# Kernel optimization log

Hardware: AMD Instinct MI355X
Metric: run time of the kernel (lower is better)

## Reference

```python
import jax, jax.numpy as jnp
import numpy as np

EPS = 1e-5

def _layernorm(x, g, b):
    mu = jnp.mean(x, axis=-1, keepdims=True)
    var = jnp.mean(jnp.square(x - mu), axis=-1, keepdims=True)
    return (x - mu) * jax.lax.rsqrt(var + EPS) * g + b

def setup_inputs() -> dict:
    key = jax.random.key(0)
    ks = jax.random.split(key, 8)
    F, N, C, H = 4096, 64, 256, 8
    x = jax.random.normal(ks[0], (F, N, C), dtype=jnp.float32)
    adj = jax.random.randint(ks[1], (N, N), 0, 2, dtype=jnp.int32)
    adj = jnp.maximum(adj, jnp.eye(N, dtype=jnp.int32))  # self-loops: no empty rows
    s = 1.0 / np.sqrt(C)
    w_qkv = jax.random.normal(ks[2], (C, 3 * C), dtype=jnp.float32) * s
    w1 = jax.random.normal(ks[3], (C, C), dtype=jnp.float32) * s
    b1 = jnp.zeros((C,), dtype=jnp.float32)
    w2 = jax.random.normal(ks[4], (C, C), dtype=jnp.float32) * s
    b2 = jnp.zeros((C,), dtype=jnp.float32)
    ln1_g = jnp.ones((C,), jnp.float32); ln1_b = jnp.zeros((C,), jnp.float32)
    ln2_g = jnp.ones((C,), jnp.float32); ln2_b = jnp.zeros((C,), jnp.float32)
    return {"x": x, "adj": adj, "w_qkv": w_qkv, "ln1_g": ln1_g, "ln1_b": ln1_b,
            "ln2_g": ln2_g, "ln2_b": ln2_b, "w1": w1, "b1": b1, "w2": w2, "b2": b2}

def reference(x, adj, w_qkv, ln1_g, ln1_b, ln2_g, ln2_b, w1, b1, w2, b2):
    F, N, C = x.shape
    H = 8
    D = C // H
    # fused QKV projection (bias-free, as in lin_qkv)
    qkv = jnp.einsum('fnc,ck->fnk', x, w_qkv)
    q, k, v = jnp.split(qkv, 3, axis=-1)
    q = q.reshape(F, N, H, D)
    k = k.reshape(F, N, H, D)
    v = v.reshape(F, N, H, D)
    # adjacency-masked attention (dropout in eval mode = identity)
    scores = jnp.einsum('fnhd,fmhd->fhnm', q, k) / jnp.sqrt(jnp.asarray(D, x.dtype))
    mask = (adj > 0)[None, None, :, :]  # [1,1,N,N]
    scores = jnp.where(mask, scores, jnp.asarray(-1e9, x.dtype))
    attn = jax.nn.softmax(scores, axis=-1)
    t = jnp.einsum('fhnm,fmhd->fnhd', attn, v).reshape(F, N, C)
    # add & norm (attention)
    x = _layernorm(x + t, ln1_g, ln1_b)
    # feed-forward: Linear -> ReLU -> Linear
    h = jax.nn.relu(jnp.einsum('fnc,cd->fnd', x, w1) + b1)
    f_out = jnp.einsum('fnd,dc->fnc', h, w2) + b2
    # add & norm (ffn)
    x = _layernorm(x + f_out, ln2_g, ln2_b)
    return x
```

## Files before the change

kernel.cpp:

```cpp
#include <hip/hip_runtime.h>
#include <hip/hip_bf16.h>

#define NN 64
#define NC 256
#define NH 8
#define ND 32

using bf16 = __hip_bfloat16;

typedef __attribute__((ext_vector_type(8))) short bf16x8v;
typedef __attribute__((ext_vector_type(4))) float f32x4;

__device__ __forceinline__ float ld(const float* p, int i) { return p[i]; }
__device__ __forceinline__ float ld(const bf16*  p, int i) { return __bfloat162float(p[i]); }

__device__ __forceinline__ unsigned short bfbits(float f) {
    bf16 h = __float2bfloat16(f);
    return *reinterpret_cast<unsigned short*>(&h);
}
__device__ __forceinline__ unsigned pack2(float lo, float hi) {
    return (unsigned)bfbits(lo) | ((unsigned)bfbits(hi) << 16);
}
__device__ __forceinline__ void st_bf16(void* p, float v) {
    *(unsigned short*)p = bfbits(v);
}
__device__ __forceinline__ float ld_lds_bf16(const void* p) {
    return __uint_as_float((unsigned)(*(const unsigned short*)p) << 16);
}
__device__ __forceinline__ f32x4 MFMA(bf16x8v a, bf16x8v b, f32x4 c) {
    return __builtin_amdgcn_mfma_f32_16x16x32_bf16(a, b, c, 0, 0, 0);
}
__device__ __forceinline__ bf16x8v LD128(const unsigned char* p) {
    return *(const bf16x8v*)p;
}

__device__ __forceinline__ int xs_chunk_byte(int r, int chunk) {
    return (r << 9) + ((chunk ^ (r & 7)) << 4);
}
__device__ __forceinline__ int xs_elem_byte(int r, int c) {
    return (r << 9) + (((c >> 3) ^ (r & 7)) << 4) + ((c & 7) << 1);
}
__device__ __forceinline__ int t128_byte(int base, int r, int chunk) {
    return base + (r << 7) + ((chunk ^ (r & 7)) << 4);
}
__device__ __forceinline__ int t64_byte(int base, int r, int chunk) {
    return base + (r << 6) + ((chunk ^ ((r >> 1) & 3)) << 4);
}
#define WBB 32768
#define VTB 45056
#define PBB 49152
#define QHB 57344
#define KHB 61440

template<typename T>
__device__ __forceinline__ void ldT2x4(const T* g, int stride, uint2& c0, uint2& c1) {
    if constexpr (sizeof(T) == 4) {
        const float* gf = (const float*)g;
        float2 r0 = *(const float2*)(gf);
        float2 r1 = *(const float2*)(gf + stride);
        float2 r2 = *(const float2*)(gf + 2 * stride);
        float2 r3 = *(const float2*)(gf + 3 * stride);
        c0.x = pack2(r0.x, r1.x); c0.y = pack2(r2.x, r3.x);
        c1.x = pack2(r0.y, r1.y); c1.y = pack2(r2.y, r3.y);
    } else {
        unsigned r0 = *(const unsigned*)(g);
        unsigned r1 = *(const unsigned*)(g + stride);
        unsigned r2 = *(const unsigned*)(g + 2 * stride);
        unsigned r3 = *(const unsigned*)(g + 3 * stride);
        c0.x = (r0 & 0xFFFFu) | (r1 << 16);
        c0.y = (r2 & 0xFFFFu) | (r3 << 16);
        c1.x = (r0 >> 16) | (r1 & 0xFFFF0000u);
        c1.y = (r2 >> 16) | (r3 & 0xFFFF0000u);
    }
}

template<typename T>
__device__ __forceinline__ void stage_wq(unsigned char* smem, const T* wqkv,
                                         int h, int k0, int tid) {
    const int jp = tid & 15;
    const int kq = (tid >> 4) * 4;
    #pragma unroll
    for (int sec = 0; sec < 3; ++sec) {
        const T* g = wqkv + (size_t)(k0 + kq) * (3 * NC) + sec * NC + h * ND + jp * 2;
        uint2 c0, c1;
        ldT2x4(g, 3 * NC, c0, c1);
        const int j = sec * 32 + jp * 2;
        const int off = (kq & 7) << 1;
        *(uint2*)(smem + t128_byte(WBB, j,     kq >> 3) + off) = c0;
        *(uint2*)(smem + t128_byte(WBB, j + 1, kq >> 3) + off) = c1;
    }
}

template<typename T>
__device__ __forceinline__ void stage_w(unsigned char* smem, const T* wm, int k0, int tid) {
    const int jp = tid & 127;
    #pragma unroll
    for (int it = 0; it < 4; ++it) {
        const int kq = (tid >> 7) * 4 + it * 8;
        const T* g = wm + (size_t)(k0 + kq) * NC + jp * 2;
        uint2 c0, c1;
        ldT2x4(g, NC, c0, c1);
        const int j = jp * 2;
        const int off = (kq & 7) << 1;
        *(uint2*)(smem + t64_byte(WBB, j,     kq >> 3) + off) = c0;
        *(uint2*)(smem + t64_byte(WBB, j + 1, kq >> 3) + off) = c1;
    }
}

template<typename T>
__device__ __forceinline__ void stage_x(unsigned char* smem, const T* xg, int tid) {
    const int r  = tid >> 2;
    const int c0 = (tid & 3) * 64;
    #pragma unroll
    for (int e = 0; e < 8; ++e) {
        const int c = c0 + e * 8;
        uint4 wv;
        if constexpr (sizeof(T) == 4) {
            const float4* g = (const float4*)((const float*)xg + r * NC + c);
            float4 v0 = g[0], v1 = g[1];
            wv.x = pack2(v0.x, v0.y); wv.y = pack2(v0.z, v0.w);
            wv.z = pack2(v1.x, v1.y); wv.w = pack2(v1.z, v1.w);
        } else {
            wv = *(const uint4*)((const bf16*)xg + r * NC + c);
        }
        *(uint4*)(smem + xs_chunk_byte(r, c >> 3)) = wv;
    }
}

__global__ void detect_dtype_kernel(const unsigned* __restrict__ g, int* __restrict__ flag) {
    *flag = (*g == 0x3F800000u) ? 1 : 0;
}

template <typename T>
__global__ __launch_bounds__(256, 2) void spatial_layer(
    const int* __restrict__ flag, const int want,
    const T* __restrict__ x, const int* __restrict__ adj,
    const T* __restrict__ wqkv,
    const T* __restrict__ ln1g, const T* __restrict__ ln1b,
    const T* __restrict__ ln2g, const T* __restrict__ ln2b,
    const T* __restrict__ w1, const T* __restrict__ fb1,
    const T* __restrict__ w2, const T* __restrict__ fb2,
    T* __restrict__ out)
{
    if (flag && *flag != want) return;

    __shared__ __align__(16) unsigned char smem[65536];

    const int tid = threadIdx.x;
    const int fr  = blockIdx.x;
    const int w   = tid >> 6;
    const int li  = tid & 15;
    const int lg  = (tid >> 4) & 3;

    {
        const uint4 zz = make_uint4(0u, 0u, 0u, 0u);
        uint4* z = (uint4*)smem;
        #pragma unroll
        for (int i = 0; i < 16; ++i) z[tid + 256 * i] = zz;
    }

    const T* xg = x + (size_t)fr * NN * NC;

    unsigned amask = 0;
    #pragma unroll
    for (int r = 0; r < 4; ++r)
        #pragma unroll
        for (int nt = 0; nt < 4; ++nt)
            if (adj[(w * 16 + lg * 4 + r) * NN + nt * 16 + li] > 0)
                amask |= 1u << (r * 4 + nt);

    __syncthreads();
    stage_x(smem, xg, tid);

    const f32x4 z4 = {0.f, 0.f, 0.f, 0.f};
    f32x4 tacc[16];
    #pragma unroll
    for (int i = 0; i < 16; ++i) tacc[i] = z4;

    #pragma unroll
    for (int h = 0; h < NH; ++h) {
        f32x4 acc6[6];
        #pragma unroll
        for (int i = 0; i < 6; ++i) acc6[i] = z4;

        #pragma unroll
        for (int s = 0; s < 4; ++s) {
            __syncthreads();
            stage_wq(smem, wqkv, h, s * 64, tid);
            __syncthreads();
            #pragma unroll
            for (int kk = 0; kk < 2; ++kk) {
                bf16x8v a = LD128(smem + xs_chunk_byte(w * 16 + li, s * 8 + kk * 4 + lg));
                #pragma unroll
                for (int nt = 0; nt < 6; ++nt) {
                    bf16x8v b = LD128(smem + t128_byte(WBB, nt * 16 + li, kk * 4 + lg));
                    acc6[nt] = MFMA(a, b, acc6[nt]);
                }
            }
        }

        #pragma unroll
        for (int nt = 0; nt < 2; ++nt)
            #pragma unroll
            for (int r = 0; r < 4; ++r) {
                const int row = w * 16 + lg * 4 + r;
                const int d   = nt * 16 + li;
                st_bf16(smem + t64_byte(QHB, row, d >> 3) + ((d & 7) << 1),
                        acc6[nt][r] * 0.17677669529663687f);
                st_bf16(smem + t64_byte(KHB, row, d >> 3) + ((d & 7) << 1),
                        acc6[2 + nt][r]);
                st_bf16(smem + t128_byte(VTB, d, row >> 3) + ((row & 7) << 1),
                        acc6[4 + nt][r]);
            }
        __syncthreads();

        {
            bf16x8v aq = LD128(smem + t64_byte(QHB, w * 16 + li, lg));
            f32x4 sc[4];
            #pragma unroll
            for (int nt = 0; nt < 4; ++nt) {
                bf16x8v bk = LD128(smem + t64_byte(KHB, nt * 16 + li, lg));
                sc[nt] = MFMA(aq, bk, z4);
            }
            #pragma unroll
            for (int r = 0; r < 4; ++r) {
                float mx = -1e30f;
                #pragma unroll
                for (int nt = 0; nt < 4; ++nt) {
                    float sv = ((amask >> (r * 4 + nt)) & 1u) ? sc[nt][r] : -1e9f;
                    sc[nt][r] = sv;
                    mx = fmaxf(mx, sv);
                }
                mx = fmaxf(mx, __shfl_xor(mx, 1));
                mx = fmaxf(mx, __shfl_xor(mx, 2));
                mx = fmaxf(mx, __shfl_xor(mx, 4));
                mx = fmaxf(mx, __shfl_xor(mx, 8));
                float sum = 0.f;
                #pragma unroll
                for (int nt = 0; nt < 4; ++nt) {
                    float e = __expf(sc[nt][r] - mx);
                    sc[nt][r] = e;
                    sum += e;
                }
                sum += __shfl_xor(sum, 1);
                sum += __shfl_xor(sum, 2);
                sum += __shfl_xor(sum, 4);
                sum += __shfl_xor(sum, 8);
                const float inv = 1.0f / sum;
                const int row = w * 16 + lg * 4 + r;
                #pragma unroll
                for (int nt = 0; nt < 4; ++nt) {
                    const int col = nt * 16 + li;
                    st_bf16(smem + t128_byte(PBB, row, col >> 3) + ((col & 7) << 1),
                            sc[nt][r] * inv);
                }
            }
        }
        __syncthreads();

        #pragma unroll
        for (int kb = 0; kb < 2; ++kb) {
            bf16x8v ap = LD128(smem + t128_byte(PBB, w * 16 + li, kb * 4 + lg));
            #pragma unroll
            for (int nt = 0; nt < 2; ++nt) {
                bf16x8v bv = LD128(smem + t128_byte(VTB, nt * 16 + li, kb * 4 + lg));
                tacc[h * 2 + nt] = MFMA(ap, bv, tacc[h * 2 + nt]);
            }
        }
    }
    __syncthreads();

    float mus[4], rss[4];
    {
        float s1[4] = {0.f, 0.f, 0.f, 0.f};
        float s2[4] = {0.f, 0.f, 0.f, 0.f};
        #pragma unroll
        for (int cb = 0; cb < 16; ++cb)
            #pragma unroll
            for (int r = 0; r < 4; ++r) {
                const int row = w * 16 + lg * 4 + r;
                const int col = cb * 16 + li;
                float y = tacc[cb][r] + ld_lds_bf16(smem + xs_elem_byte(row, col));
                tacc[cb][r] = y;
                s1[r] += y; s2[r] += y * y;
            }
        #pragma unroll
        for (int r = 0; r < 4; ++r) {
            float a = s1[r], b = s2[r];
            a += __shfl_xor(a, 1); b += __shfl_xor(b, 1);
            a += __shfl_xor(a, 2); b += __shfl_xor(b, 2);
            a += __shfl_xor(a, 4); b += __shfl_xor(b, 4);
            a += __shfl_xor(a, 8); b += __shfl_xor(b, 8);
            const float mu  = a * (1.f / 256.f);
            const float var = b * (1.f / 256.f) - mu * mu;
            mus[r] = mu;
            rss[r] = rsqrtf(var + 1e-5f);
        }
        #pragma unroll
        for (int cb = 0; cb < 16; ++cb) {
            const int col = cb * 16 + li;
            const float g = ld(ln1g, col), be = ld(ln1b, col);
            #pragma unroll
            for (int r = 0; r < 4; ++r) {
                const int row = w * 16 + lg * 4 + r;
                const float x1 = (tacc[cb][r] - mus[r]) * rss[r] * g + be;
                tacc[cb][r] = x1;
                st_bf16(smem + xs_elem_byte(row, col), x1);
            }
        }
    }

    f32x4 facc[16];
    #pragma unroll
    for (int i = 0; i < 16; ++i) facc[i] = z4;
    #pragma unroll
    for (int s = 0; s < 8; ++s) {
        __syncthreads();
        stage_w(smem, w1, s * 32, tid);
        __syncthreads();
        bf16x8v a = LD128(smem + xs_chunk_byte(w * 16 + li, s * 4 + lg));
        #pragma unroll
        for (int nt = 0; nt < 16; ++nt) {
            bf16x8v b = LD128(smem + t64_byte(WBB, nt * 16 + li, lg));
            facc[nt] = MFMA(a, b, facc[nt]);
        }
    }
    #pragma unroll
    for (int nt = 0; nt < 16; ++nt) {
        const int col = nt * 16 + li;
        const float bv = ld(fb1, col);
        #pragma unroll
        for (int r = 0; r < 4; ++r) {
            const int row = w * 16 + lg * 4 + r;
            st_bf16(smem + xs_elem_byte(row, col), fmaxf(facc[nt][r] + bv, 0.f));
        }
    }

    #pragma unroll
    for (int i = 0; i < 16; ++i) facc[i] = z4;
    #pragma unroll
    for (int s = 0; s < 8; ++s) {
        __syncthreads();
        stage_w(smem, w2, s * 32, tid);
        __syncthreads();
        bf16x8v a = LD128(smem + xs_chunk_byte(w * 16 + li, s * 4 + lg));
        #pragma unroll
        for (int nt = 0; nt < 16; ++nt) {
            bf16x8v b = LD128(smem + t64_byte(WBB, nt * 16 + li, lg));
            facc[nt] = MFMA(a, b, facc[nt]);
        }
    }

    {
        float s1[4] = {0.f, 0.f, 0.f, 0.f};
        float s2[4] = {0.f, 0.f, 0.f, 0.f};
        #pragma unroll
        for (int cb = 0; cb < 16; ++cb) {
            const float bv = ld(fb2, cb * 16 + li);
            #pragma unroll
            for (int r = 0; r < 4; ++r) {
                const float y = tacc[cb][r] + facc[cb][r] + bv;
                facc[cb][r] = y;
                s1[r] += y; s2[r] += y * y;
            }
        }
        #pragma unroll
        for (int r = 0; r < 4; ++r) {
            float a = s1[r], b = s2[r];
            a += __shfl_xor(a, 1); b += __shfl_xor(b, 1);
            a += __shfl_xor(a, 2); b += __shfl_xor(b, 2);
            a += __shfl_xor(a, 4); b += __shfl_xor(b, 4);
            a += __shfl_xor(a, 8); b += __shfl_xor(b, 8);
            const float mu  = a * (1.f / 256.f);
            const float var = b * (1.f / 256.f) - mu * mu;
            mus[r] = mu;
            rss[r] = rsqrtf(var + 1e-5f);
        }
        T* og = out + (size_t)fr * NN * NC;
        #pragma unroll
        for (int cb = 0; cb < 16; ++cb) {
            const int col = cb * 16 + li;
            const float g = ld(ln2g, col), be = ld(ln2b, col);
            #pragma unroll
            for (int r = 0; r < 4; ++r) {
                const int row = w * 16 + lg * 4 + r;
                const float yv = (facc[cb][r] - mus[r]) * rss[r] * g + be;
                if constexpr (sizeof(T) == 4) ((float*)og)[row * NC + col] = yv;
                else ((unsigned short*)og)[row * NC + col] = bfbits(yv);
            }
        }
    }
}

extern "C" void kernel_launch(void* const* d_in, const int* in_sizes, int n_in,
                              void* d_out, int out_size, void* d_ws, size_t ws_size,
                              hipStream_t stream) {
    const int F = in_sizes[0] / (NN * NC);

    const int* flag = (ws_size >= 4) ? (const int*)d_ws : nullptr;
    if (flag) {
        detect_dtype_kernel<<<1, 1, 0, stream>>>((const unsigned*)d_in[3], (int*)d_ws);
        spatial_layer<bf16><<<dim3(F), dim3(256), 0, stream>>>(
            flag, 0,
            (const bf16*)d_in[0], (const int*)d_in[1], (const bf16*)d_in[2],
            (const bf16*)d_in[3], (const bf16*)d_in[4],
            (const bf16*)d_in[5], (const bf16*)d_in[6],
            (const bf16*)d_in[7], (const bf16*)d_in[8],
            (const bf16*)d_in[9], (const bf16*)d_in[10],
            (bf16*)d_out);
    }
    spatial_layer<float><<<dim3(F), dim3(256), 0, stream>>>(
        flag, 1,
        (const float*)d_in[0], (const int*)d_in[1], (const float*)d_in[2],
        (const float*)d_in[3], (const float*)d_in[4],
        (const float*)d_in[5], (const float*)d_in[6],
        (const float*)d_in[7], (const float*)d_in[8],
        (const float*)d_in[9], (const float*)d_in[10],
        (float*)d_out);
}
```

Baseline: 1.427 ms.

## Double-buffer weight staging via register prefetch and keep x fragments in registers

Weight tiles for the QKV, FFN1 and FFN2 GEMMs are now loaded from global memory into registers one stage ahead and written into a second LDS buffer after the MFMAs. This overlaps global latency with compute and halves the barriers per stage. The x A-operand fragments and the residual x values are held in registers instead of an LDS tile, which frees LDS for the two weight buffers. The final output is staged through LDS so each thread writes vectorized, coalesced 16-byte stores. In exchange, register pressure rises a lot (xa, xres, rq/rw, tacc, facc) and may spill or reduce occupancy.

```diff
diff --git a/kernel.cpp b/kernel.cpp
--- a/kernel.cpp
+++ b/kernel.cpp
@@ -24,9 +24,8 @@
 __device__ __forceinline__ void st_bf16(void* p, float v) {
     *(unsigned short*)p = bfbits(v);
 }
-__device__ __forceinline__ float ld_lds_bf16(const void* p) {
-    return __uint_as_float((unsigned)(*(const unsigned short*)p) << 16);
-}
+__device__ __forceinline__ float lo2f(unsigned p) { return __uint_as_float(p << 16); }
+__device__ __forceinline__ float hi2f(unsigned p) { return __uint_as_float(p & 0xffff0000u); }
 __device__ __forceinline__ f32x4 MFMA(bf16x8v a, bf16x8v b, f32x4 c) {
     return __builtin_amdgcn_mfma_f32_16x16x32_bf16(a, b, c, 0, 0, 0);
 }
@@ -34,96 +33,122 @@
     return *(const bf16x8v*)p;
 }
 
-__device__ __forceinline__ int xs_chunk_byte(int r, int chunk) {
-    return (r << 9) + ((chunk ^ (r & 7)) << 4);
-}
-__device__ __forceinline__ int xs_elem_byte(int r, int c) {
-    return (r << 9) + (((c >> 3) ^ (r & 7)) << 4) + ((c & 7) << 1);
-}
 __device__ __forceinline__ int t128_byte(int base, int r, int chunk) {
     return base + (r << 7) + ((chunk ^ (r & 7)) << 4);
 }
 __device__ __forceinline__ int t64_byte(int base, int r, int chunk) {
     return base + (r << 6) + ((chunk ^ ((r >> 1) & 3)) << 4);
 }
-#define WBB 32768
-#define VTB 45056
-#define PBB 49152
-#define QHB 57344
-#define KHB 61440
+#define WB(i) ((i) << 14)
+#define VTB 32768
+#define PBB 36864
+#define QHB 45056
+#define KHB 49152
+#define XS2 32768
+__device__ __forceinline__ int xs2_chunk(int r, int c) {
+    return XS2 + (r << 9) + ((c ^ (r & 7)) << 4);
+}
+__device__ __forceinline__ int xs2_elem(int r, int c) {
+    return XS2 + (r << 9) + (((c >> 3) ^ (r & 7)) << 4) + ((c & 7) << 1);
+}
+__device__ __forceinline__ int yf_byte(int r, int c16) {
+    return (r << 10) + ((c16 ^ (r & 7)) << 4);
+}
+
+template<int S> struct RawSel { using type = unsigned; };
+template<> struct RawSel<4>   { using type = float2;   };
+template<typename T> using RawW = typename RawSel<sizeof(T)>::type;
 
 template<typename T>
-__device__ __forceinline__ void ldT2x4(const T* g, int stride, uint2& c0, uint2& c1) {
+__device__ __forceinline__ void raw_load4(const T* g, int stride, RawW<T>* r) {
     if constexpr (sizeof(T) == 4) {
         const float* gf = (const float*)g;
-        float2 r0 = *(const float2*)(gf);
-        float2 r1 = *(const float2*)(gf + stride);
-        float2 r2 = *(const float2*)(gf + 2 * stride);
-        float2 r3 = *(const float2*)(gf + 3 * stride);
-        c0.x = pack2(r0.x, r1.x); c0.y = pack2(r2.x, r3.x);
-        c1.x = pack2(r0.y, r1.y); c1.y = pack2(r2.y, r3.y);
+        r[0] = *(const float2*)(gf);
+        r[1] = *(const float2*)(gf + stride);
+        r[2] = *(const float2*)(gf + 2 * stride);
+        r[3] = *(const float2*)(gf + 3 * stride);
     } else {
-        unsigned r0 = *(const unsigned*)(g);
-        unsigned r1 = *(const unsigned*)(g + stride);
-        unsigned r2 = *(const unsigned*)(g + 2 * stride);
-        unsigned r3 = *(const unsigned*)(g + 3 * stride);
-        c0.x = (r0 & 0xFFFFu) | (r1 << 16);
-        c0.y = (r2 & 0xFFFFu) | (r3 << 16);
-        c1.x = (r0 >> 16) | (r1 & 0xFFFF0000u);
-        c1.y = (r2 >> 16) | (r3 & 0xFFFF0000u);
-    }
+        r[0] = *(const unsigned*)(g);
+        r[1] = *(const unsigned*)(g + stride);
+        r[2] = *(const unsigned*)(g + 2 * stride);
+        r[3] = *(const unsigned*)(g + 3 * stride);
+    }
+}
+__device__ __forceinline__ void raw_pack(const float2* r, uint2& c0, uint2& c1) {
+    c0.x = pack2(r[0].x, r[1].x); c0.y = pack2(r[2].x, r[3].x);
+    c1.x = pack2(r[0].y, r[1].y); c1.y = pack2(r[2].y, r[3].y);
+}
+__device__ __forceinline__ void raw_pack(const unsigned* r, uint2& c0, uint2& c1) {
+    c0.x = (r[0] & 0xFFFFu) | (r[1] << 16);
+    c0.y = (r[2] & 0xFFFFu) | (r[3] << 16);
+    c1.x = (r[0] >> 16) | (r[1] & 0xFFFF0000u);
+    c1.y = (r[2] >> 16) | (r[3] & 0xFFFF0000u);
 }
 
 template<typename T>
-__device__ __forceinline__ void stage_wq(unsigned char* smem, const T* wqkv,
-                                         int h, int k0, int tid) {
+__device__ __forceinline__ void wq_load(const T* wqkv, int h, int k0, int tid, RawW<T>* rv) {
     const int jp = tid & 15;
     const int kq = (tid >> 4) * 4;
     #pragma unroll
+    for (int sec = 0; sec < 3; ++sec)
+        raw_load4(wqkv + (size_t)(k0 + kq) * (3 * NC) + sec * NC + h * ND + jp * 2,
+                  3 * NC, rv + sec * 4);
+}
+template<typename T>
+__device__ __forceinline__ void wq_store(unsigned char* smem, int wb, int tid, const RawW<T>* rv) {
+    const int jp = tid & 15;
+    const int kq = (tid >> 4) * 4;
+    const int off = (kq & 7) << 1;
+    #pragma unroll
     for (int sec = 0; sec < 3; ++sec) {
-        const T* g = wqkv + (size_t)(k0 + kq) * (3 * NC) + sec * NC + h * ND + jp * 2;
         uint2 c0, c1;
-        ldT2x4(g, 3 * NC, c0, c1);
+        raw_pack(rv + sec * 4, c0, c1);
         const int j = sec * 32 + jp * 2;
-        const int off = (kq & 7) << 1;
-        *(uint2*)(smem + t128_byte(WBB, j,     kq >> 3) + off) = c0;
-        *(uint2*)(smem + t128_byte(WBB, j + 1, kq >> 3) + off) = c1;
+        *(uint2*)(smem + t128_byte(wb, j,     kq >> 3) + off) = c0;
+        *(uint2*)(smem + t128_byte(wb, j + 1, kq >> 3) + off) = c1;
     }
 }
 
 template<typename T>
-__device__ __forceinline__ void stage_w(unsigned char* smem, const T* wm, int k0, int tid) {
+__device__ __forceinline__ void w_load(const T* wm, int k0, int tid, RawW<T>* rv) {
     const int jp = tid & 127;
     #pragma unroll
     for (int it = 0; it < 4; ++it) {
         const int kq = (tid >> 7) * 4 + it * 8;
-        const T* g = wm + (size_t)(k0 + kq) * NC + jp * 2;
+        raw_load4(wm + (size_t)(k0 + kq) * NC + jp * 2, NC, rv + it * 4);
+    }
+}
+template<typename T>
+__device__ __forceinline__ void w_store(unsigned char* smem, int wb, int tid, const RawW<T>* rv) {
+    const int jp = tid & 127;
+    #pragma unroll
+    for (int it = 0; it < 4; ++it) {
         uint2 c0, c1;
-        ldT2x4(g, NC, c0, c1);
+        raw_pack(rv + it * 4, c0, c1);
+        const int kq = (tid >> 7) * 4 + it * 8;
         const int j = jp * 2;
         const int off = (kq & 7) << 1;
-        *(uint2*)(smem + t64_byte(WBB, j,     kq >> 3) + off) = c0;
-        *(uint2*)(smem + t64_byte(WBB, j + 1, kq >> 3) + off) = c1;
+        *(uint2*)(smem + t64_byte(wb, j,     kq >> 3) + off) = c0;
+        *(uint2*)(smem + t64_byte(wb, j + 1, kq >> 3) + off) = c1;
     }
 }
 
 template<typename T>
-__device__ __forceinline__ void stage_x(unsigned char* smem, const T* xg, int tid) {
-    const int r  = tid >> 2;
-    const int c0 = (tid & 3) * 64;
-    #pragma unroll
-    for (int e = 0; e < 8; ++e) {
-        const int c = c0 + e * 8;
-        uint4 wv;
+__device__ __forceinline__ void xa_load(const T* xg, int row, int lg, bf16x8v* xa) {
+    #pragma unroll
+    for (int j = 0; j < 8; ++j) {
+        const int k = (lg + 4 * j) * 8;
         if constexpr (sizeof(T) == 4) {
-            const float4* g = (const float4*)((const float*)xg + r * NC + c);
+            const float4* g = (const float4*)((const float*)xg + row * NC + k);
             float4 v0 = g[0], v1 = g[1];
-            wv.x = pack2(v0.x, v0.y); wv.y = pack2(v0.z, v0.w);
-            wv.z = pack2(v1.x, v1.y); wv.w = pack2(v1.z, v1.w);
+            uint4 u;
+            u.x = pack2(v0.x, v0.y); u.y = pack2(v0.z, v0.w);
+            u.z = pack2(v1.x, v1.y); u.w = pack2(v1.z, v1.w);
+            bf16x8v t; *(uint4*)&t = u;
+            xa[j] = t;
         } else {
-            wv = *(const uint4*)((const bf16*)xg + r * NC + c);
-        }
-        *(uint4*)(smem + xs_chunk_byte(r, c >> 3)) = wv;
+            xa[j] = *(const bf16x8v*)((const bf16*)xg + row * NC + k);
+        }
     }
 }
 
@@ -152,31 +177,49 @@
     const int li  = tid & 15;
     const int lg  = (tid >> 4) & 3;
 
+    const T* xg = x + (size_t)fr * NN * NC;
+
+    bf16x8v xa[8];
+    xa_load(xg, w * 16 + li, lg, xa);
+
+    RawW<T> rq[12];
+    wq_load(wqkv, 0, 0, tid, rq);
+
+    unsigned amask = 0;
+    #pragma unroll
+    for (int r = 0; r < 4; ++r)
+        #pragma unroll
+        for (int nt = 0; nt < 4; ++nt)
+            if (adj[(w * 16 + lg * 4 + r) * NN + nt * 16 + li] > 0)
+                amask |= 1u << (r * 4 + nt);
+
+    unsigned xres[32];
+    #pragma unroll
+    for (int cb = 0; cb < 16; ++cb)
+        #pragma unroll
+        for (int rp = 0; rp < 2; ++rp) {
+            float a0 = ld(xg, (w * 16 + lg * 4 + rp * 2    ) * NC + cb * 16 + li);
+            float a1 = ld(xg, (w * 16 + lg * 4 + rp * 2 + 1) * NC + cb * 16 + li);
+            xres[cb * 2 + rp] = pack2(a0, a1);
+        }
+
     {
         const uint4 zz = make_uint4(0u, 0u, 0u, 0u);
         uint4* z = (uint4*)smem;
         #pragma unroll
         for (int i = 0; i < 16; ++i) z[tid + 256 * i] = zz;
     }
-
-    const T* xg = x + (size_t)fr * NN * NC;
-
-    unsigned amask = 0;
-    #pragma unroll
-    for (int r = 0; r < 4; ++r)
-        #pragma unroll
-        for (int nt = 0; nt < 4; ++nt)
-            if (adj[(w * 16 + lg * 4 + r) * NN + nt * 16 + li] > 0)
-                amask |= 1u << (r * 4 + nt);
-
     __syncthreads();
-    stage_x(smem, xg, tid);
+    wq_store<T>(smem, WB(0), tid, rq);
+    __syncthreads();
 
     const f32x4 z4 = {0.f, 0.f, 0.f, 0.f};
     f32x4 tacc[16];
     #pragma unroll
     for (int i = 0; i < 16; ++i) tacc[i] = z4;
 
+    RawW<T> rw[16];
+
     #pragma unroll
     for (int h = 0; h < NH; ++h) {
         f32x4 acc6[6];
@@ -185,18 +228,23 @@
 
         #pragma unroll
         for (int s = 0; s < 4; ++s) {
-            __syncthreads();
-            stage_wq(smem, wqkv, h, s * 64, tid);
-            __syncthreads();
+            const int cur = s & 1;
+            const bool have_next = (h < NH - 1) || (s < 3);
+            if (have_next)
+                wq_load(wqkv, (s == 3) ? h + 1 : h, (s == 3) ? 0 : (s + 1) * 64, tid, rq);
+            else
+                w_load(w1, 0, tid, rw);
             #pragma unroll
             for (int kk = 0; kk < 2; ++kk) {
-                bf16x8v a = LD128(smem + xs_chunk_byte(w * 16 + li, s * 8 + kk * 4 + lg));
+                bf16x8v a = xa[s * 2 + kk];
                 #pragma unroll
                 for (int nt = 0; nt < 6; ++nt) {
-                    bf16x8v b = LD128(smem + t128_byte(WBB, nt * 16 + li, kk * 4 + lg));
+                    bf16x8v b = LD128(smem + t128_byte(WB(cur), nt * 16 + li, kk * 4 + lg));
                     acc6[nt] = MFMA(a, b, acc6[nt]);
                 }
             }
+            if (have_next) wq_store<T>(smem, WB(cur ^ 1), tid, rq);
+            if (s < 3) __syncthreads();
         }
 
         #pragma unroll
@@ -270,6 +318,8 @@
     }
     __syncthreads();
 
+    w_store<T>(smem, WB(0), tid, rw);
+
     float mus[4], rss[4];
     {
         float s1[4] = {0.f, 0.f, 0.f, 0.f};
@@ -278,9 +328,8 @@
         for (int cb = 0; cb < 16; ++cb)
             #pragma unroll
             for (int r = 0; r < 4; ++r) {
-                const int row = w * 16 + lg * 4 + r;
-                const int col = cb * 16 + li;
-                float y = tacc[cb][r] + ld_lds_bf16(smem + xs_elem_byte(row, col));
+                unsigned p = xres[cb * 2 + (r >> 1)];
+                float y = tacc[cb][r] + ((r & 1) ? hi2f(p) : lo2f(p));
                 tacc[cb][r] = y;
                 s1[r] += y; s2[r] += y * y;
             }
@@ -305,26 +354,30 @@
                 const int row = w * 16 + lg * 4 + r;
                 const float x1 = (tacc[cb][r] - mus[r]) * rss[r] * g + be;
                 tacc[cb][r] = x1;
-                st_bf16(smem + xs_elem_byte(row, col), x1);
-            }
-        }
-    }
+                st_bf16(smem + xs2_elem(row, col), x1);
+            }
+        }
+    }
+    __syncthreads();
 
     f32x4 facc[16];
     #pragma unroll
     for (int i = 0; i < 16; ++i) facc[i] = z4;
     #pragma unroll
     for (int s = 0; s < 8; ++s) {
+        const int cur = s & 1;
+        if (s < 7) w_load(w1, (s + 1) * 32, tid, rw);
+        else       w_load(w2, 0, tid, rw);
+        bf16x8v a = LD128(smem + xs2_chunk(w * 16 + li, s * 4 + lg));
+        #pragma unroll
+        for (int nt = 0; nt < 16; ++nt) {
+            bf16x8v b = LD128(smem + t64_byte(WB(cur), nt * 16 + li, lg));
+            facc[nt] = MFMA(a, b, facc[nt]);
+        }
+        w_store<T>(smem, WB(cur ^ 1), tid, rw);
         __syncthreads();
-        stage_w(smem, w1, s * 32, tid);
-        __syncthreads();
-        bf16x8v a = LD128(smem + xs_chunk_byte(w * 16 + li, s * 4 + lg));
-        #pragma unroll
-        for (int nt = 0; nt < 16; ++nt) {
-            bf16x8v b = LD128(smem + t64_byte(WBB, nt * 16 + li, lg));
-            facc[nt] = MFMA(a, b, facc[nt]);
-        }
-    }
+    }
+
     #pragma unroll
     for (int nt = 0; nt < 16; ++nt) {
         const int col = nt * 16 + li;
@@ -332,7 +385,7 @@
         #pragma unroll
         for (int r = 0; r < 4; ++r) {
             const int row = w * 16 + lg * 4 + r;
-            st_bf16(smem + xs_elem_byte(row, col), fmaxf(facc[nt][r] + bv, 0.f));
+            st_bf16(smem + xs2_elem(row, col), fmaxf(facc[nt][r] + bv, 0.f));
         }
     }
 
@@ -340,16 +393,17 @@
     for (int i = 0; i < 16; ++i) facc[i] = z4;
     #pragma unroll
     for (int s = 0; s < 8; ++s) {
-        __syncthreads();
-        stage_w(smem, w2, s * 32, tid);
-        __syncthreads();
-        bf16x8v a = LD128(smem + xs_chunk_byte(w * 16 + li, s * 4 + lg));
+        const int cur = s & 1;
+        if (s < 7) w_load(w2, (s + 1) * 32, tid, rw);
+        bf16x8v a = LD128(smem + xs2_chunk(w * 16 + li, s * 4 + lg));
         #pragma unroll
         for (int nt = 0; nt < 16; ++nt) {
-            bf16x8v b = LD128(smem + t64_byte(WBB, nt * 16 + li, lg));
+            bf16x8v b = LD128(smem + t64_byte(WB(cur), nt * 16 + li, lg));
             facc[nt] = MFMA(a, b, facc[nt]);
         }
-    }
+        if (s < 7) { w_store<T>(smem, WB(cur ^ 1), tid, rw); __syncthreads(); }
+    }
+    __syncthreads();
 
     {
         float s1[4] = {0.f, 0.f, 0.f, 0.f};
@@ -376,17 +430,44 @@
             mus[r] = mu;
             rss[r] = rsqrtf(var + 1e-5f);
         }
-        T* og = out + (size_t)fr * NN * NC;
-        #pragma unroll
-        for (int cb = 0; cb < 16; ++cb) {
-            const int col = cb * 16 + li;
-            const float g = ld(ln2g, col), be = ld(ln2b, col);
-            #pragma unroll
-            for (int r = 0; r < 4; ++r) {
-                const int row = w * 16 + lg * 4 + r;
-                const float yv = (facc[cb][r] - mus[r]) * rss[r] * g + be;
-                if constexpr (sizeof(T) == 4) ((float*)og)[row * NC + col] = yv;
-                else ((unsigned short*)og)[row * NC + col] = bfbits(yv);
+
+        if constexpr (sizeof(T) == 4) {
+            #pragma unroll
+            for (int cb = 0; cb < 16; ++cb) {
+                const int col = cb * 16 + li;
+                const float g = ld(ln2g, col), be = ld(ln2b, col);
+                #pragma unroll
+                for (int r = 0; r < 4; ++r) {
+                    const int row = w * 16 + lg * 4 + r;
+                    *(float*)(smem + yf_byte(row, col >> 2) + ((col & 3) << 2)) =
+                        (facc[cb][r] - mus[r]) * rss[r] * g + be;
+                }
+            }
+            const int rr = tid >> 2, cb16 = (tid & 3) * 16;
+            float4* og4 = (float4*)((float*)out + (size_t)fr * NN * NC);
+            #pragma unroll
+            for (int i = 0; i < 16; ++i) {
+                float4 v = *(const float4*)(smem + yf_byte(rr, cb16 + i));
+                og4[rr * 64 + (tid & 3) * 16 + i] = v;
+            }
+        } else {
+            #pragma unroll
+            for (int cb = 0; cb < 16; ++cb) {
+                const int col = cb * 16 + li;
+                const float g = ld(ln2g, col), be = ld(ln2b, col);
+                #pragma unroll
+                for (int r = 0; r < 4; ++r) {
+                    const int row = w * 16 + lg * 4 + r;
+                    st_bf16(smem + xs2_elem(row, col),
+                            (facc[cb][r] - mus[r]) * rss[r] * g + be);
+                }
+            }
+            const int rr = tid >> 2;
+            int4* og4 = (int4*)(out + (size_t)fr * NN * NC);
+            #pragma unroll
+            for (int i = 0; i < 8; ++i) {
+                int4 v = *(const int4*)(smem + xs2_chunk(rr, (tid & 3) * 8 + i));
+                og4[rr * 32 + (tid & 3) * 8 + i] = v;
             }
         }
     }
```

Measured after the change: 2.088 ms. 1.46x slower.
